# Kernel tuning notes

Measured on AMD Instinct MI355X. Metric: run time of the kernel, lower is better.

The kernel has to match this reference:

```python
import jax, jax.numpy as jnp
import numpy as np

B, S, HID = 2, 2048, 2048
NH, DN, DR, DV, RANK = 16, 128, 64, 128, 512
DQK = DN + DR
SCALE = DQK ** -0.5
EPS = 1e-5


def _rope(x, theta):
    # x: [..., d] with d even; theta broadcastable to [..., d//2] (angle per pair)
    x1, x2 = x[..., 0::2], x[..., 1::2]
    c, s = jnp.cos(theta), jnp.sin(theta)
    return jnp.stack([x1 * c - x2 * s, x1 * s + x2 * c], axis=-1).reshape(x.shape)


def _layernorm(x, gamma, beta):
    mu = jnp.mean(x, axis=-1, keepdims=True)
    var = jnp.var(x, axis=-1, keepdims=True)
    return (x - mu) * jax.lax.rsqrt(var + EPS) * gamma + beta


def setup_inputs() -> dict:
    key = jax.random.key(0)
    ks = jax.random.split(key, 8)
    def xavier(k, fan_in, fan_out, gain=1.0):
        lim = gain * np.sqrt(6.0 / (fan_in + fan_out))
        return jax.random.uniform(k, (fan_in, fan_out), jnp.float32, -lim, lim)
    return {
        "hidden_states": jax.random.normal(ks[0], (B, S, HID), jnp.float32),
        "freqs_cis": jax.random.uniform(ks[1], (S, DR // 2), jnp.float32) * 2.0 * np.pi,
        "Wq": xavier(ks[2], HID, NH * DQK),                      # q_proj (stored [in,out])
        "Wkv_a": xavier(ks[3], HID, RANK + DR),                  # kv_proj_a
        "kv_gamma": jnp.ones((RANK,), jnp.float32),              # kv_norm
        "kv_beta": jnp.zeros((RANK,), jnp.float32),
        "Wkv_b": xavier(ks[4], RANK, NH * (DN + DV)),            # kv_proj_b
        "Wout": xavier(ks[5], NH * DV, HID, gain=1.0 / np.sqrt(2.0)),  # out_proj
    }


def reference(hidden_states, freqs_cis, Wq, Wkv_a, kv_gamma, kv_beta, Wkv_b, Wout):
    b, s, _ = hidden_states.shape
    max_len = freqs_cis.shape[0]
    pos = jnp.arange(s) % max_len                      # [s], position_ids=None path
    theta = freqs_cis[pos]                             # [s, DR//2]

    # Q projection, split nope/rope, partial RoPE
    q = (hidden_states @ Wq).reshape(b, s, NH, DQK)
    q_nope, q_rope = q[..., :DN], q[..., DN:]
    q_rope = _rope(q_rope, theta[None, :, None, :])    # [b,s,nh,DR]

    # Low-rank KV: compressed latent + shared rope key
    kv = hidden_states @ Wkv_a                         # [b,s,RANK+DR]
    kv_c, k_rope = kv[..., :RANK], kv[..., RANK:]
    k_rope = _rope(k_rope, theta[None, :, :])          # [b,s,DR]
    kv_c = _layernorm(kv_c, kv_gamma, kv_beta)
    kvb = (kv_c @ Wkv_b).reshape(b, s, NH, DN + DV)
    k_nope, v = kvb[..., :DN], kvb[..., DN:]
    k = jnp.concatenate(
        [k_nope, jnp.broadcast_to(k_rope[:, :, None, :], (b, s, NH, DR))], axis=-1)

    q = jnp.concatenate([q_nope, q_rope], axis=-1)     # [b,s,nh,DQK]
    scores = jnp.einsum('bthd,bshd->btsh', q, k) * SCALE
    weights = jax.nn.softmax(scores.astype(jnp.float32), axis=2).astype(q.dtype)
    attn = jnp.einsum('btsh,bshd->bthd', weights, v).reshape(b, s, NH * DV)
    return attn @ Wout
```

## Files before the change

### kernel.cpp

```cpp
#include <hip/hip_runtime.h>

#define BATCH 2
#define SEQ   2048
#define HID   2048
#define NH    16
#define DN    128
#define DR    64
#define DV    128
#define RANK  512
#define DQK   192
#define NQ    (NH*DQK)
#define NQKV  3712
#define NKVB  (NH*(DN+DV))
#define NTOK  (BATCH*SEQ)
#define SCALE_F 0.07216878364870323f
#define SCALE_LOG2E 0.10411754831420211f

typedef __bf16 bf16x8 __attribute__((ext_vector_type(8)));
typedef float  f32x4  __attribute__((ext_vector_type(4)));
typedef unsigned int u32x4 __attribute__((ext_vector_type(4)));
typedef unsigned short u16;
typedef unsigned short u16x4 __attribute__((ext_vector_type(4)));

__device__ __forceinline__ float b2f(u16 h) {
    unsigned int u = ((unsigned int)h) << 16;
    float f; __builtin_memcpy(&f, &u, 4); return f;
}
__device__ __forceinline__ u16 f2b(float f) {
    unsigned int x; __builtin_memcpy(&x, &f, 4);
    unsigned int r = x + 0x7fffu + ((x >> 16) & 1u);
    return (u16)(r >> 16);
}
__device__ __forceinline__ bf16x8 lds_frag(const u16* p) {
    u32x4 v = *(const u32x4*)p;
    return __builtin_bit_cast(bf16x8, v);
}
__device__ __forceinline__ bf16x8 to_frag(u32x4 v) {
    return __builtin_bit_cast(bf16x8, v);
}
__device__ __forceinline__ f32x4 mfma16(bf16x8 a, bf16x8 b, f32x4 c) {
    return __builtin_amdgcn_mfma_f32_16x16x32_bf16(a, b, c, 0, 0, 0);
}
__device__ __forceinline__ void store_out(u16* p, float v) { *p = f2b(v); }
__device__ __forceinline__ void store_out(float* p, float v) { *p = v; }
__device__ __forceinline__ void gld_lds16(const u16* g, u16* l) {
    __builtin_amdgcn_global_load_lds(
        (const __attribute__((address_space(1))) unsigned int*)g,
        (__attribute__((address_space(3))) unsigned int*)l, 16, 0, 0);
}

__global__ __launch_bounds__(256) void prep_kernel(
        const float* __restrict__ hs_f, u16* __restrict__ hs,
        const float* __restrict__ Wq, const float* __restrict__ Wkva,
        const float* __restrict__ Wkvb, const float* __restrict__ Wout,
        u16* __restrict__ WqkvT, u16* __restrict__ WkvbT, u16* __restrict__ WoutT) {
    int tid = threadIdx.x;
    int bid = blockIdx.x;
    if (bid < 8192) {
        int i = bid * 256 + tid;
        f32x4 v = *(const f32x4*)(hs_f + (size_t)i * 4);
        u16 o[4];
        for (int k = 0; k < 4; k++) o[k] = f2b(v[k]);
        *(unsigned long long*)(hs + (size_t)i * 4) = *(unsigned long long*)o;
        return;
    }
    bid -= 8192;
    const float* in; u16* out; int R, C, tilesC;
    if (bid < 1536)      { in = Wq;   out = WqkvT;                       R = HID;  C = NQ;   tilesC = 48; }
    else if (bid < 1856) { bid -= 1536; in = Wkva; out = WqkvT + (size_t)NQ * HID; R = HID; C = 576; tilesC = 10; }
    else if (bid < 2368) { bid -= 1856; in = Wkvb; out = WkvbT;          R = RANK; C = NKVB; tilesC = 64; }
    else                 { bid -= 2368; in = Wout; out = WoutT;          R = HID;  C = HID;  tilesC = 32; }
    __shared__ unsigned int t32[64 * 65];
    int r0 = (bid / tilesC) * 64, c0 = (bid % tilesC) * 64;
    bool valid = (c0 < C);
    for (int i = 0; i < 4; i++) {
        int u = tid + i * 256;
        int rl = u >> 4, c4 = u & 15;
        f32x4 v = {0.f, 0.f, 0.f, 0.f};
        if (valid) v = *(const f32x4*)&in[(size_t)(r0 + rl) * C + c0 + c4 * 4];
        for (int j = 0; j < 4; j++)
            t32[(c4 * 4 + j) * 65 + rl] = f2b(v[j]);
    }
    __syncthreads();
    for (int i = 0; i < 2; i++) {
        int u = tid + i * 256;
        int cl = u >> 3, r8 = (u & 7) * 8;
        unsigned int w[8];
        for (int j = 0; j < 8; j++) w[j] = t32[cl * 65 + r8 + j];
        u32x4 pk;
        for (int j = 0; j < 4; j++) pk[j] = (w[2 * j] & 0xffffu) | (w[2 * j + 1] << 16);
        *(u32x4*)&out[(size_t)(c0 + cl) * R + r0 + r8] = pk;
    }
}

template <typename OutT>
__global__ __launch_bounds__(256) void gemm_bt(const u16* __restrict__ A,
                                               const u16* __restrict__ Bt,
                                               OutT* __restrict__ C,
                                               int K, int lda, int ldb, int ldc) {
    __shared__ u16 As[128 * 32];
    __shared__ u16 Bs[128 * 32];
    int tid = threadIdx.x, lane = tid & 63, w = tid >> 6;
    int wm = (w >> 1) * 64, wn = (w & 1) * 64;
    int g = lane >> 4, ln = lane & 15;
    int m0 = blockIdx.y * 128, n0 = blockIdx.x * 128;
    f32x4 acc[4][4] = {};
    for (int k0 = 0; k0 < K; k0 += 32) {
        for (int i = 0; i < 2; i++) {
            int ch = tid + i * 256;
            int row = ch >> 2, o = ch & 3;
            gld_lds16(&A[(size_t)(m0 + row) * lda + k0 + o * 8], &As[row * 32 + o * 8]);
            gld_lds16(&Bt[(size_t)(n0 + row) * ldb + k0 + o * 8], &Bs[row * 32 + o * 8]);
        }
        __syncthreads();
        bf16x8 af[4], bf[4];
        for (int i = 0; i < 4; i++) af[i] = lds_frag(&As[(wm + i * 16 + ln) * 32 + g * 8]);
        for (int j = 0; j < 4; j++) bf[j] = lds_frag(&Bs[(wn + j * 16 + ln) * 32 + g * 8]);
        for (int i = 0; i < 4; i++)
            for (int j = 0; j < 4; j++)
                acc[i][j] = mfma16(af[i], bf[j], acc[i][j]);
        __syncthreads();
    }
    for (int i = 0; i < 4; i++)
        for (int j = 0; j < 4; j++)
            for (int r = 0; r < 4; r++) {
                int m = m0 + wm + i * 16 + g * 4 + r;
                int n = n0 + wn + j * 16 + ln;
                store_out(&C[(size_t)m * ldc + n], acc[i][j][r]);
            }
}

__global__ void rope_q(u16* __restrict__ qkv, const float* __restrict__ freqs) {
    int token = blockIdx.x;
    int s = token & (SEQ - 1);
    int tid = threadIdx.x;
    for (int i = 0; i < 2; i++) {
        int idx = tid + i * 256;
        int hh = idx >> 5, p = idx & 31;
        float th = freqs[s * 32 + p];
        float c = __cosf(th), sn = __sinf(th);
        size_t off = (size_t)token * NQKV + hh * DQK + DN + 2 * p;
        float x1 = b2f(qkv[off]), x2 = b2f(qkv[off + 1]);
        qkv[off]     = f2b(x1 * c - x2 * sn);
        qkv[off + 1] = f2b(x1 * sn + x2 * c);
    }
}

__global__ void ln_kv(const u16* __restrict__ qkv, const float* __restrict__ gamma,
                      const float* __restrict__ beta, u16* __restrict__ kv_c) {
    int row = blockIdx.x, tid = threadIdx.x;
    size_t base = (size_t)row * NQKV + NQ;
    float x0 = b2f(qkv[base + tid]), x1 = b2f(qkv[base + 256 + tid]);
    float s = x0 + x1, q2 = x0 * x0 + x1 * x1;
    for (int o = 32; o > 0; o >>= 1) { s += __shfl_xor(s, o); q2 += __shfl_xor(q2, o); }
    __shared__ float sh[8];
    int lane = tid & 63, w = tid >> 6;
    if (lane == 0) { sh[w] = s; sh[4 + w] = q2; }
    __syncthreads();
    float S = sh[0] + sh[1] + sh[2] + sh[3];
    float Q2 = sh[4] + sh[5] + sh[6] + sh[7];
    float mu = S * (1.f / 512.f);
    float var = Q2 * (1.f / 512.f) - mu * mu;
    float rs = rsqrtf(var + 1e-5f);
    kv_c[(size_t)row * RANK + tid] =
        f2b((x0 - mu) * rs * gamma[tid] + beta[tid]);
    kv_c[(size_t)row * RANK + 256 + tid] =
        f2b((x1 - mu) * rs * gamma[256 + tid] + beta[256 + tid]);
}

__global__ void k_assemble(const u16* __restrict__ kvb, const u16* __restrict__ qkv,
                           const float* __restrict__ freqs, u16* __restrict__ Kf) {
    int token = blockIdx.x;
    int b = token >> 11;
    int s = token & (SEQ - 1);
    int tid = threadIdx.x;
    __shared__ u16 roped[64];
    if (tid < 32) {
        int p = tid;
        float th = freqs[s * 32 + p];
        float c = __cosf(th), sn = __sinf(th);
        float x1 = b2f(qkv[(size_t)token * NQKV + NQ + RANK + 2 * p]);
        float x2 = b2f(qkv[(size_t)token * NQKV + NQ + RANK + 2 * p + 1]);
        roped[2 * p]     = f2b(x1 * c - x2 * sn);
        roped[2 * p + 1] = f2b(x1 * sn + x2 * c);
    }
    __syncthreads();
    int kt = s >> 6, r = s & 63;
    int swr = ((r >> 1) & 3) * 8;
    {
        int hh = tid >> 4, c8 = (tid & 15) * 8;
        size_t dst = ((size_t)(b * NH + hh) * 32 + kt) * 12288
                   + (size_t)(c8 >> 5) * 2048 + r * 32 + ((c8 & 31) ^ swr);
        *(u32x4*)&Kf[dst] = *(const u32x4*)&kvb[(size_t)token * NKVB + hh * 256 + c8];
    }
    if (tid < 128) {
        int hh = tid >> 3, c8 = (tid & 7) * 8;
        size_t dst = ((size_t)(b * NH + hh) * 32 + kt) * 12288
                   + (size_t)(4 + (c8 >> 5)) * 2048 + r * 32 + ((c8 & 31) ^ swr);
        *(u32x4*)&Kf[dst] = *(u32x4*)&roped[c8];
    }
}

__global__ void v_transpose(const u16* __restrict__ kvb, u16* __restrict__ Vt) {
    __shared__ unsigned int t32[64 * 65];
    int bx = blockIdx.x;
    int st = bx * 64, dt = blockIdx.y * 64;
    int b = blockIdx.z >> 4, h = blockIdx.z & 15;
    int tid = threadIdx.x;
    for (int i = 0; i < 2; i++) {
        int u = tid + i * 256;
        int sl = u >> 3, c8 = (u & 7) * 8;
        u32x4 v = *(const u32x4*)&kvb[((size_t)(b * SEQ + st + sl) * NH + h) * 256 + DN + dt + c8];
        for (int j = 0; j < 4; j++) {
            t32[(c8 + 2 * j) * 65 + sl]     = v[j] & 0xffffu;
            t32[(c8 + 2 * j + 1) * 65 + sl] = v[j] >> 16;
        }
    }
    __syncthreads();
    for (int i = 0; i < 2; i++) {
        int u = tid + i * 256;
        int dl = u >> 3, s8 = (u & 7) * 8;
        unsigned int w[8];
        for (int j = 0; j < 8; j++) w[j] = t32[dl * 65 + s8 + j];
        u32x4 pk;
        for (int j = 0; j < 4; j++) pk[j] = (w[2 * j] & 0xffffu) | (w[2 * j + 1] << 16);
        size_t dst = ((size_t)(b * NH + h) * 32 + bx) * 8192
                   + (size_t)(s8 >> 5) * 4096 + (size_t)(dt + dl) * 32 + (s8 & 31);
        *(u32x4*)&Vt[dst] = pk;
    }
}

#define KC    64
#define QTILE 64
#define NIT  (SEQ / KC)
__global__ __launch_bounds__(256, 4) void attn_kernel(const u16* __restrict__ Q,
                                                      const u16* __restrict__ Kf,
                                                      const u16* __restrict__ Vt,
                                                      u16* __restrict__ O) {
    __shared__ u16 Ks[6 * 64 * 32];
    __shared__ u16 Ps[2][QTILE * 64];
    int tid = threadIdx.x, lane = tid & 63, w = tid >> 6;
    int w1 = w & 1;
    int w2 = w >> 1;
    int g = lane >> 4, ln = lane & 15;
    int bid = blockIdx.x;
    int swz = ((bid & 7) << 7) | (bid >> 3);
    int qt = swz & 31, h = (swz >> 5) & 15, b = swz >> 9;

    size_t qbase = ((size_t)(b * SEQ + qt * QTILE)) * NQKV + h * DQK;
    const u16* Kh = Kf + (size_t)(b * NH + h) * (32 * 12288);
    const u16* Vh = Vt + (size_t)(b * NH + h) * (32 * 8192);

    u32x4 qreg[2][6];
#pragma unroll
    for (int ni = 0; ni < 2; ni++)
#pragma unroll
        for (int kk = 0; kk < 6; kk++) {
            const u16* qp = &Q[qbase + (size_t)(w1 * 32 + ni * 16 + ln) * NQKV + kk * 32 + g * 8];
            asm volatile("global_load_dwordx4 %0, %1, off"
                         : "=v"(qreg[ni][kk]) : "v"(qp));
        }
#pragma unroll
    for (int i = 0; i < 6; i++)
        gld_lds16(&Kh[i * 2048 + tid * 8], &Ks[i * 2048 + tid * 8]);

    int kRd0 = (w2 * 32 + ln) * 64 + ((g * 16) ^ (((ln >> 1) & 3) << 4));
    int kRd1 = kRd0 + 16 * 64;
    int vrow = w2 * 2048 + ln * 32 + g * 8;
    int pswz = (ln & 7) << 4;

    f32x4 oacc[2][4] = {};
    float lpriv[2] = {0.f, 0.f};

    for (int kt = 0; kt < NIT; kt++) {
        asm volatile("s_waitcnt vmcnt(0)" ::: "memory");
        __builtin_amdgcn_sched_barrier(0);
        __syncthreads();
        const char* KsB = (const char*)Ks;
        f32x4 sacc[2][2] = {};
#pragma unroll
        for (int kk = 0; kk < 6; kk++) {
            bf16x8 af0 = lds_frag((const u16*)(KsB + kk * 4096 + kRd0));
            bf16x8 af1 = lds_frag((const u16*)(KsB + kk * 4096 + kRd1));
            bf16x8 q0 = to_frag(qreg[0][kk]), q1 = to_frag(qreg[1][kk]);
            sacc[0][0] = mfma16(af0, q0, sacc[0][0]);
            sacc[0][1] = mfma16(af0, q1, sacc[0][1]);
            sacc[1][0] = mfma16(af1, q0, sacc[1][0]);
            sacc[1][1] = mfma16(af1, q1, sacc[1][1]);
        }
        char* Pb = (char*)Ps[kt & 1];
#pragma unroll
        for (int mi = 0; mi < 2; mi++)
#pragma unroll
            for (int ni = 0; ni < 2; ni++) {
                float p0 = exp2f(sacc[mi][ni][0] * SCALE_LOG2E);
                float p1 = exp2f(sacc[mi][ni][1] * SCALE_LOG2E);
                float p2 = exp2f(sacc[mi][ni][2] * SCALE_LOG2E);
                float p3 = exp2f(sacc[mi][ni][3] * SCALE_LOG2E);
                lpriv[ni] += (p0 + p1) + (p2 + p3);
                unsigned int c0, c1;
                asm("v_cvt_pk_bf16_f32 %0, %1, %2" : "=v"(c0) : "v"(p0), "v"(p1));
                asm("v_cvt_pk_bf16_f32 %0, %1, %2" : "=v"(c1) : "v"(p2), "v"(p3));
                uint2 pk; pk.x = c0; pk.y = c1;
                int pwB = (w1 * 32 + ni * 16 + ln) * 128
                        + ((w2 * 64 + mi * 32 + g * 8) ^ pswz);
                *(uint2*)(Pb + pwB) = pk;
            }
        __syncthreads();
        if (kt + 1 < NIT) {
            const u16* kT = Kh + (size_t)(kt + 1) * 12288;
#pragma unroll
            for (int i = 0; i < 6; i++)
                gld_lds16(&kT[i * 2048 + tid * 8], &Ks[i * 2048 + tid * 8]);
        }
        const u16* vT = Vh + (size_t)kt * 8192;
#pragma unroll
        for (int kk = 0; kk < 2; kk++) {
            bf16x8 pa[2], vb[4];
#pragma unroll
            for (int mi = 0; mi < 2; mi++)
                pa[mi] = lds_frag((const u16*)(Pb + (w1 * 32 + mi * 16 + ln) * 128
                                               + ((kk * 64 + g * 16) ^ pswz)));
#pragma unroll
            for (int ni = 0; ni < 4; ni++)
                vb[ni] = to_frag(*(const u32x4*)&vT[kk * 4096 + ni * 512 + vrow]);
#pragma unroll
            for (int mi = 0; mi < 2; mi++)
#pragma unroll
                for (int ni = 0; ni < 4; ni++)
                    oacc[mi][ni] = mfma16(pa[mi], vb[ni], oacc[mi][ni]);
        }
    }

    float* lsumF = (float*)Ps[0];
    for (int ni = 0; ni < 2; ni++) {
        float v = lpriv[ni];
        v += __shfl_xor(v, 16);
        v += __shfl_xor(v, 32);
        if (g == 0) lsumF[w2 * 64 + w1 * 32 + ni * 16 + ln] = v;
    }
    __syncthreads();
    for (int mi = 0; mi < 2; mi++)
        for (int ni = 0; ni < 4; ni++) {
            int d = w2 * 64 + ni * 16 + ln;
            for (int r = 0; r < 4; r++) {
                int row = w1 * 32 + mi * 16 + g * 4 + r;
                float l = lsumF[row] + lsumF[64 + row];
                O[((size_t)(b * SEQ + qt * QTILE + row) * NH + h) * DV + d] =
                    f2b(oacc[mi][ni][r] / l);
            }
        }
}

extern "C" void kernel_launch(void* const* d_in, const int* in_sizes, int n_in,
                              void* d_out, int out_size, void* d_ws, size_t ws_size,
                              hipStream_t stream) {
    const float* hs_f  = (const float*)d_in[0];
    const float* freqs = (const float*)d_in[1];
    const float* Wq    = (const float*)d_in[2];
    const float* Wkva  = (const float*)d_in[3];
    const float* gamma = (const float*)d_in[4];
    const float* beta  = (const float*)d_in[5];
    const float* Wkvb  = (const float*)d_in[6];
    const float* Wout  = (const float*)d_in[7];
    float* outp = (float*)d_out;

    char* ws = (char*)d_ws;
    size_t off = 0;
    auto alloc = [&](size_t elems) -> u16* {
        u16* p = (u16*)(ws + off);
        off += ((elems * 2 + 255) / 256) * 256;
        return p;
    };
    u16* hs     = alloc((size_t)NTOK * HID);
    u16* WqkvT  = alloc((size_t)NQKV * HID);
    u16* WkvbT  = alloc((size_t)NKVB * RANK);
    u16* WoutT  = alloc((size_t)HID * HID);
    u16* qkv    = alloc((size_t)NTOK * NQKV);
    u16* kv_c   = alloc((size_t)NTOK * RANK);
    u16* kvb    = alloc((size_t)NTOK * NKVB);
    u16* Kf     = alloc((size_t)NTOK * NQ);
    u16* Vt     = alloc((size_t)BATCH * NH * DV * SEQ);
    u16* attn   = alloc((size_t)NTOK * NH * DV);
    (void)ws_size; (void)in_sizes; (void)n_in; (void)out_size;

    prep_kernel<<<8192 + 1536 + 320 + 512 + 1024, 256, 0, stream>>>(
        hs_f, hs, Wq, Wkva, Wkvb, Wout, WqkvT, WkvbT, WoutT);

    gemm_bt<<<dim3(NQKV / 128, NTOK / 128), 256, 0, stream>>>(hs, WqkvT, qkv, HID, HID, HID, NQKV);

    rope_q<<<NTOK, 256, 0, stream>>>(qkv, freqs);

    ln_kv<<<NTOK, 256, 0, stream>>>(qkv, gamma, beta, kv_c);

    gemm_bt<<<dim3(NKVB / 128, NTOK / 128), 256, 0, stream>>>(kv_c, WkvbT, kvb, RANK, RANK, RANK, NKVB);

    k_assemble<<<NTOK, 256, 0, stream>>>(kvb, qkv, freqs, Kf);

    v_transpose<<<dim3(SEQ / 64, DV / 64, BATCH * NH), 256, 0, stream>>>(kvb, Vt);

    attn_kernel<<<1024, 256, 0, stream>>>(qkv, Kf, Vt, attn);

    gemm_bt<<<dim3(HID / 128, NTOK / 128), 256, 0, stream>>>(attn, WoutT, outp, HID, HID, HID, HID);
}
```

Before: 479.8 us.

## Add 256x256-tile double-buffered swizzled GEMM for QKV and KV-b projections

Introduces a new 512-thread GEMM kernel with 256x256 output tiles, BK=64, XOR-swizzled LDS staging, double buffering that prefetches the next K tile while MFMAs run, and s_setprio around the MFMA phases. It replaces the 128x128 gemm_bt for the fused QKV projection and the kv_b projection. NQKV is padded to 3840 so that dimension divides into 256-wide tiles, and the weight-prep grid gains extra zero-filled tiles to cover the padding. The goal is more data reuse per LDS load and load latency hidden behind compute. The cost is heavy register and LDS use, and fewer blocks (e.g. 15x16 for QKV), which risks under-filling the GPU's CUs.

```diff
diff --git a/kernel.cpp b/kernel.cpp
--- a/kernel.cpp
+++ b/kernel.cpp
@@ -10,7 +10,7 @@
 #define RANK  512
 #define DQK   192
 #define NQ    (NH*DQK)
-#define NQKV  3712
+#define NQKV  3840
 #define NKVB  (NH*(DN+DV))
 #define NTOK  (BATCH*SEQ)
 #define SCALE_F 0.07216878364870323f
@@ -67,9 +67,9 @@
     bid -= 8192;
     const float* in; u16* out; int R, C, tilesC;
     if (bid < 1536)      { in = Wq;   out = WqkvT;                       R = HID;  C = NQ;   tilesC = 48; }
-    else if (bid < 1856) { bid -= 1536; in = Wkva; out = WqkvT + (size_t)NQ * HID; R = HID; C = 576; tilesC = 10; }
-    else if (bid < 2368) { bid -= 1856; in = Wkvb; out = WkvbT;          R = RANK; C = NKVB; tilesC = 64; }
-    else                 { bid -= 2368; in = Wout; out = WoutT;          R = HID;  C = HID;  tilesC = 32; }
+    else if (bid < 1920) { bid -= 1536; in = Wkva; out = WqkvT + (size_t)NQ * HID; R = HID; C = 576; tilesC = 12; }
+    else if (bid < 2432) { bid -= 1920; in = Wkvb; out = WkvbT;          R = RANK; C = NKVB; tilesC = 64; }
+    else                 { bid -= 2432; in = Wout; out = WoutT;          R = HID;  C = HID;  tilesC = 32; }
     __shared__ unsigned int t32[64 * 65];
     int r0 = (bid / tilesC) * 64, c0 = (bid % tilesC) * 64;
     bool valid = (c0 < C);
@@ -127,6 +127,138 @@
                 int m = m0 + wm + i * 16 + g * 4 + r;
                 int n = n0 + wn + j * 16 + ln;
                 store_out(&C[(size_t)m * ldc + n], acc[i][j][r]);
+            }
+}
+
+template <typename OutT>
+__global__ __launch_bounds__(512, 2) void gemm256(const u16* __restrict__ A,
+                                                  const u16* __restrict__ Bt,
+                                                  OutT* __restrict__ C,
+                                                  int K, int lda, int ldb, int ldc) {
+    __shared__ u16 lds[8][128 * 64];
+    int tid = threadIdx.x, lane = tid & 63, w = tid >> 6;
+    int wm = w >> 2, wn = w & 3;
+    int g = lane >> 4, ln = lane & 15;
+    int m0 = blockIdx.y * 256, n0 = blockIdx.x * 256;
+
+    int srow = tid >> 3, schunk = tid & 7;
+    int cs = schunk ^ (srow & 7);
+    int sdst = tid * 8;
+
+    auto stage = [&](int p, int ht, int t) {
+        const u16* src = (ht < 2) ? A : Bt;
+        int ld = (ht < 2) ? lda : ldb;
+        int base = ((ht < 2) ? m0 : n0) + (ht & 1) * 128;
+        u16* buf = lds[p * 4 + ht];
+        int k0 = t << 6;
+        gld_lds16(&src[(size_t)(base + srow) * ld + k0 + cs * 8], &buf[sdst]);
+        gld_lds16(&src[(size_t)(base + 64 + srow) * ld + k0 + cs * 8], &buf[4096 + sdst]);
+    };
+
+    int aR = ln * 64;
+    int ck0 = ((g ^ (ln & 7)) << 3);
+    int ck1 = (((4 + g) ^ (ln & 7)) << 3);
+    int bB = (wn & 1) * 4096;
+
+    f32x4 acc[8][4] = {};
+    int NT = K >> 6;
+
+    for (int ht = 0; ht < 4; ht++) stage(0, ht, 0);
+    __builtin_amdgcn_sched_barrier(0);
+    asm volatile("s_waitcnt vmcnt(0)" ::: "memory");
+    __builtin_amdgcn_sched_barrier(0);
+    __builtin_amdgcn_s_barrier();
+
+    for (int t = 0; t < NT; t++) {
+        const u16* Ab = lds[(t & 1) * 4 + wm];
+        const u16* Bb = lds[(t & 1) * 4 + 2 + (wn >> 1)];
+        int pn = (t & 1) ^ 1;
+        bool pf = (t + 1 < NT);
+        bf16x8 af[4][2], bf[4][2];
+
+#pragma unroll
+        for (int f = 0; f < 4; f++) {
+            af[f][0] = lds_frag(&Ab[f * 1024 + aR + ck0]);
+            af[f][1] = lds_frag(&Ab[f * 1024 + aR + ck1]);
+        }
+#pragma unroll
+        for (int nf = 0; nf < 2; nf++) {
+            bf[nf][0] = lds_frag(&Bb[bB + nf * 1024 + aR + ck0]);
+            bf[nf][1] = lds_frag(&Bb[bB + nf * 1024 + aR + ck1]);
+        }
+        if (pf) { stage(pn, 0, t + 1); stage(pn, 1, t + 1); }
+        __builtin_amdgcn_s_barrier();
+        __builtin_amdgcn_s_setprio(1);
+#pragma unroll
+        for (int f = 0; f < 4; f++)
+#pragma unroll
+            for (int nf = 0; nf < 2; nf++) {
+                acc[f][nf] = mfma16(af[f][0], bf[nf][0], acc[f][nf]);
+                acc[f][nf] = mfma16(af[f][1], bf[nf][1], acc[f][nf]);
+            }
+        __builtin_amdgcn_s_setprio(0);
+
+#pragma unroll
+        for (int nf = 2; nf < 4; nf++) {
+            bf[nf][0] = lds_frag(&Bb[bB + nf * 1024 + aR + ck0]);
+            bf[nf][1] = lds_frag(&Bb[bB + nf * 1024 + aR + ck1]);
+        }
+        if (pf) { stage(pn, 2, t + 1); stage(pn, 3, t + 1); }
+        __builtin_amdgcn_s_barrier();
+        __builtin_amdgcn_s_setprio(1);
+#pragma unroll
+        for (int f = 0; f < 4; f++)
+#pragma unroll
+            for (int nf = 2; nf < 4; nf++) {
+                acc[f][nf] = mfma16(af[f][0], bf[nf][0], acc[f][nf]);
+                acc[f][nf] = mfma16(af[f][1], bf[nf][1], acc[f][nf]);
+            }
+        __builtin_amdgcn_s_setprio(0);
+
+#pragma unroll
+        for (int f = 0; f < 4; f++) {
+            af[f][0] = lds_frag(&Ab[(f + 4) * 1024 + aR + ck0]);
+            af[f][1] = lds_frag(&Ab[(f + 4) * 1024 + aR + ck1]);
+        }
+        __builtin_amdgcn_s_barrier();
+        __builtin_amdgcn_s_setprio(1);
+#pragma unroll
+        for (int f = 0; f < 4; f++)
+#pragma unroll
+            for (int nf = 0; nf < 2; nf++) {
+                acc[f + 4][nf] = mfma16(af[f][0], bf[nf][0], acc[f + 4][nf]);
+                acc[f + 4][nf] = mfma16(af[f][1], bf[nf][1], acc[f + 4][nf]);
+            }
+        __builtin_amdgcn_s_setprio(0);
+
+        __builtin_amdgcn_s_barrier();
+        __builtin_amdgcn_s_setprio(1);
+#pragma unroll
+        for (int f = 0; f < 4; f++)
+#pragma unroll
+            for (int nf = 2; nf < 4; nf++) {
+                acc[f + 4][nf] = mfma16(af[f][0], bf[nf][0], acc[f + 4][nf]);
+                acc[f + 4][nf] = mfma16(af[f][1], bf[nf][1], acc[f + 4][nf]);
+            }
+        __builtin_amdgcn_s_setprio(0);
+
+        if (pf) {
+            __builtin_amdgcn_sched_barrier(0);
+            asm volatile("s_waitcnt vmcnt(0)" ::: "memory");
+            __builtin_amdgcn_sched_barrier(0);
+            __builtin_amdgcn_s_barrier();
+        }
+    }
+
+#pragma unroll
+    for (int f = 0; f < 8; f++)
+#pragma unroll
+        for (int nf = 0; nf < 4; nf++)
+#pragma unroll
+            for (int r = 0; r < 4; r++) {
+                int m = m0 + wm * 128 + f * 16 + g * 4 + r;
+                int n = n0 + wn * 64 + nf * 16 + ln;
+                store_out(&C[(size_t)m * ldc + n], acc[f][nf][r]);
             }
 }
 
@@ -384,16 +516,16 @@
     u16* attn   = alloc((size_t)NTOK * NH * DV);
     (void)ws_size; (void)in_sizes; (void)n_in; (void)out_size;
 
-    prep_kernel<<<8192 + 1536 + 320 + 512 + 1024, 256, 0, stream>>>(
+    prep_kernel<<<8192 + 1536 + 384 + 512 + 1024, 256, 0, stream>>>(
         hs_f, hs, Wq, Wkva, Wkvb, Wout, WqkvT, WkvbT, WoutT);
 
-    gemm_bt<<<dim3(NQKV / 128, NTOK / 128), 256, 0, stream>>>(hs, WqkvT, qkv, HID, HID, HID, NQKV);
+    gemm256<<<dim3(NQKV / 256, NTOK / 256), 512, 0, stream>>>(hs, WqkvT, qkv, HID, HID, HID, NQKV);
 
     rope_q<<<NTOK, 256, 0, stream>>>(qkv, freqs);
 
     ln_kv<<<NTOK, 256, 0, stream>>>(qkv, gamma, beta, kv_c);
 
-    gemm_bt<<<dim3(NKVB / 128, NTOK / 128), 256, 0, stream>>>(kv_c, WkvbT, kvb, RANK, RANK, RANK, NKVB);
+    gemm256<<<dim3(NKVB / 256, NTOK / 256), 512, 0, stream>>>(kv_c, WkvbT, kvb, RANK, RANK, RANK, NKVB);
 
     k_assemble<<<NTOK, 256, 0, stream>>>(kvb, qkv, freqs, Kf);
 
```

New measurement: 421.9 us. -12.1%, faster.
